# Kernel optimization log

Measured on AMD Instinct MI355X. Metric: run time of the kernel, lower is better.

Reference implementation:

```python
import jax, jax.numpy as jnp
import numpy as np

BN_EPS = 1e-5


def setup_inputs() -> dict:
    key = jax.random.key(0)
    ks = jax.random.split(key, 16)
    N, E, IN, H, A, L = 50000, 400000, 128, 192, 192, 3
    s = 0.02
    inp = {
        "x": jax.random.normal(ks[0], (N, IN), dtype=jnp.float32),
        "edge_index": jax.random.randint(ks[1], (2, E), 0, N, dtype=jnp.int32),
        "seed_idx": 123,
        "proj_w": jax.random.normal(ks[2], (IN, H), dtype=jnp.float32) * s,
        "proj_b": jnp.zeros((H,), dtype=jnp.float32),
        "mlp1_w": jax.random.normal(ks[3], (L, H, H), dtype=jnp.float32) * s,
        "mlp1_b": jnp.zeros((L, H), dtype=jnp.float32),
        "mlp2_w": jax.random.normal(ks[4], (L, H, H), dtype=jnp.float32) * s,
        "mlp2_b": jnp.zeros((L, H), dtype=jnp.float32),
        "eps": jnp.zeros((L,), dtype=jnp.float32),  # GIN train_eps init 0
        "bn_g": jnp.ones((L, H), dtype=jnp.float32),
        "bn_b": jnp.zeros((L, H), dtype=jnp.float32),
        "W1": jax.random.normal(ks[5], (H, A), dtype=jnp.float32) * s,
        "W2": jax.random.normal(ks[6], (H, A), dtype=jnp.float32) * s,
        "w_attn": jax.random.normal(ks[7], (A,), dtype=jnp.float32) * s,
        "cls_w": jax.random.normal(ks[8], (H,), dtype=jnp.float32) * s,
        "cls_b": jnp.zeros((1,), dtype=jnp.float32),
    }
    return inp


def _forward(x, edge_index, seed_idx, proj_w, proj_b, mlp1_w, mlp1_b,
             mlp2_w, mlp2_b, eps, bn_g, bn_b, W1, W2, w_attn, cls_w, cls_b):
    N = x.shape[0]
    src, dst = edge_index[0], edge_index[1]
    h = jax.nn.relu(x @ proj_w + proj_b)  # [N, H]
    L = mlp1_w.shape[0]
    for l in range(L):
        # GINConv: mlp((1+eps)*h + sum_{j->i} h_j) via scatter-add on dst
        agg = jax.ops.segment_sum(h[src], dst, num_segments=N)  # [N, H]
        z = (1.0 + eps[l]) * h + agg
        z = jax.nn.relu(z @ mlp1_w[l] + mlp1_b[l]) @ mlp2_w[l] + mlp2_b[l]
        # BatchNorm over nodes (batch statistics)
        mu = z.mean(axis=0)
        var = z.var(axis=0)
        z = (z - mu) * jax.lax.rsqrt(var + BN_EPS) * bn_g[l] + bn_b[l]
        h = jax.nn.relu(z)  # dropout is identity in eval
    h_seed = h[seed_idx]  # valid seed index branch
    zat = jnp.tanh(h @ W1 + h_seed @ W2)          # [N, A]
    e = jax.nn.leaky_relu(zat @ w_attn, 0.2)      # [N]
    alpha = jax.nn.softmax(e, axis=0)             # [N]
    readout = alpha @ h                           # [H]
    logit = readout @ cls_w + cls_b               # [1]
    return logit, alpha


def reference(x, edge_index, seed_idx, proj_w, proj_b, mlp1_w, mlp1_b,
              mlp2_w, mlp2_b, eps, bn_g, bn_b, W1, W2, w_attn, cls_w, cls_b):
    return _forward(x, edge_index, seed_idx, proj_w, proj_b, mlp1_w, mlp1_b,
                    mlp2_w, mlp2_b, eps, bn_g, bn_b, W1, W2, w_attn, cls_w, cls_b)
```

## Files before the change

kernel.cpp:

```cpp
#include <hip/hip_runtime.h>
#include <hip/hip_bf16.h>

#define N_NODES 50000
#define N_EDGES 400000
#define DIM_IN  128
#define DIM_H   192
#define N_LAYERS 3
#define BN_EPSF 1e-5f
#define SCAN_NBLK 49
#define INV_N (1.f / N_NODES)
#define NSHADOW 8
#define SSTRIDE 384
#define WTP_BLOCKS 138

typedef __attribute__((ext_vector_type(8))) short short8;
typedef __attribute__((ext_vector_type(4))) float floatx4;

union FragU { uint4 u; short8 s; };

__device__ __forceinline__ float relu_f(float x) { return x > 0.f ? x : 0.f; }
__device__ __forceinline__ unsigned short f2bf(float x) {
  __hip_bfloat16 h = __float2bfloat16(x);
  return *reinterpret_cast<unsigned short*>(&h);
}
__device__ __forceinline__ float bf2f(unsigned short b) {
  return __uint_as_float(((unsigned)b) << 16);
}
__device__ __forceinline__ float bflo(unsigned u) { return __uint_as_float(u << 16); }
__device__ __forceinline__ float bfhi(unsigned u) { return __uint_as_float(u & 0xffff0000u); }

__device__ __forceinline__ unsigned char f2f8(float v) {
  return (unsigned char)(__builtin_amdgcn_cvt_pk_fp8_f32(v, v, 0, false) & 0xff);
}
template <int SEL>
__device__ __forceinline__ float f8dec(unsigned u) {
  return __builtin_amdgcn_cvt_f32_fp8((int)u, SEL);
}

__global__ void k_wtp_hist(const float* __restrict__ m1, const float* __restrict__ m2,
                           const float* __restrict__ wa, const float* __restrict__ pw,
                           uint4* __restrict__ outp,
                           const int* __restrict__ edge, int* __restrict__ cnt) {
  if (blockIdx.x < WTP_BLOCKS) {
    const int NH = 7 * 24 * 192;
    const int NP = 16 * 192;
    int idx = blockIdx.x * 256 + threadIdx.x;
    if (idx >= NH + NP) return;
    union { uint4 u; unsigned short h[8]; } fr;
    if (idx < NH) {
      int mat = idx / (24 * 192);
      int rem = idx - mat * (24 * 192);
      int kidx = rem / 192, col = rem - kidx * 192;
      const float* src = mat < 3 ? m1 + (size_t)mat * (DIM_H * DIM_H)
                       : (mat < 6 ? m2 + (size_t)(mat - 3) * (DIM_H * DIM_H) : wa);
#pragma unroll
      for (int t = 0; t < 8; ++t) fr.h[t] = f2bf(src[(size_t)(kidx * 8 + t) * DIM_H + col]);
    } else {
      int rem = idx - NH;
      int kidx = rem / 192, col = rem - kidx * 192;
#pragma unroll
      for (int t = 0; t < 8; ++t) fr.h[t] = f2bf(pw[(size_t)(kidx * 8 + t) * DIM_H + col]);
    }
    outp[idx] = fr.u;
  } else {
    int e = (blockIdx.x - WTP_BLOCKS) * 256 + threadIdx.x;
    if (e < N_EDGES) atomicAdd(&cnt[edge[N_EDGES + e]], 1);
  }
}

__global__ void k_scanA(const int* __restrict__ deg, int* __restrict__ part, int* __restrict__ bsum) {
  __shared__ int buf[1024];
  int g = blockIdx.x * 1024 + threadIdx.x;
  int v = (g < N_NODES) ? deg[g] : 0;
  buf[threadIdx.x] = v;
  __syncthreads();
  for (int off = 1; off < 1024; off <<= 1) {
    int t = (threadIdx.x >= off) ? buf[threadIdx.x - off] : 0;
    __syncthreads();
    buf[threadIdx.x] += t;
    __syncthreads();
  }
  if (g < N_NODES) part[g] = buf[threadIdx.x];
  if (threadIdx.x == 1023) bsum[blockIdx.x] = buf[1023];
}

__global__ void k_scanC(const int* __restrict__ part, const int* __restrict__ bsum,
                        int* __restrict__ rowptr, int* __restrict__ cursor) {
  __shared__ int excl[64];
  int tid = threadIdx.x;
  if (tid < 64) {
    int own = (tid < SCAN_NBLK) ? bsum[tid] : 0;
    int v = own;
    for (int off = 1; off < 64; off <<= 1) {
      int t = __shfl_up(v, off);
      if (tid >= off) v += t;
    }
    excl[tid] = v - own;
  }
  __syncthreads();
  int g = blockIdx.x * 256 + tid;
  if (g == 0) { rowptr[0] = 0; cursor[0] = 0; }
  if (g < N_NODES) {
    int v = part[g] + excl[g >> 10];
    rowptr[g + 1] = v;
    if (g + 1 < N_NODES) cursor[g + 1] = v;
  }
}

__global__ void k_fill(const int* __restrict__ edge, int* __restrict__ cursor, int* __restrict__ csr) {
  int e = blockIdx.x * 256 + threadIdx.x;
  if (e < N_EDGES) {
    int s = edge[e];
    int d = edge[N_EDGES + e];
    int pos = atomicAdd(&cursor[d], 1);
    csr[pos] = s;
  }
}

template <bool BN>
__global__ void k_agg(const unsigned char* __restrict__ z, const int* __restrict__ rowptr,
                      const int* __restrict__ csr, const float* __restrict__ stats,
                      const float* __restrict__ bng, const float* __restrict__ bnb,
                      const float* __restrict__ eps, int l, unsigned short* __restrict__ outA) {
  int wid = threadIdx.x >> 6, lane = threadIdx.x & 63;
  int node = blockIdx.x * 4 + wid;
  if (node >= N_NODES || lane >= 48) return;
  int c = lane * 4;
  float4 sc4 = {1.f, 1.f, 1.f, 1.f}, sh4 = {0.f, 0.f, 0.f, 0.f};
  if (BN) {
    float4 st = {0.f, 0.f, 0.f, 0.f}, sq = {0.f, 0.f, 0.f, 0.f};
#pragma unroll
    for (int g = 0; g < NSHADOW; ++g) {
      const float* sp = stats + g * SSTRIDE;
      float4 a = *(const float4*)(sp + c);
      float4 b = *(const float4*)(sp + DIM_H + c);
      st.x += a.x; st.y += a.y; st.z += a.z; st.w += a.w;
      sq.x += b.x; sq.y += b.y; sq.z += b.z; sq.w += b.w;
    }
    float4 g4 = *(const float4*)(bng + c);
    float4 b4 = *(const float4*)(bnb + c);
    float mu, rs;
    mu = st.x * INV_N; rs = rsqrtf(sq.x * INV_N - mu * mu + BN_EPSF); sc4.x = g4.x * rs; sh4.x = b4.x - mu * sc4.x;
    mu = st.y * INV_N; rs = rsqrtf(sq.y * INV_N - mu * mu + BN_EPSF); sc4.y = g4.y * rs; sh4.y = b4.y - mu * sc4.y;
    mu = st.z * INV_N; rs = rsqrtf(sq.z * INV_N - mu * mu + BN_EPSF); sc4.z = g4.z * rs; sh4.z = b4.z - mu * sc4.z;
    mu = st.w * INV_N; rs = rsqrtf(sq.w * INV_N - mu * mu + BN_EPSF); sc4.w = g4.w * rs; sh4.w = b4.w - mu * sc4.w;
  }
  float a0 = 0.f, a1 = 0.f, a2 = 0.f, a3 = 0.f;
  int beg = rowptr[node], end = rowptr[node + 1];
  unsigned us = *(const unsigned*)(z + (size_t)node * DIM_H + c);
#define ACCU(U)                                                          \
  {                                                                      \
    float v0 = f8dec<0>(U), v1 = f8dec<1>(U);                            \
    float v2 = f8dec<2>(U), v3 = f8dec<3>(U);                            \
    if (BN) {                                                            \
      v0 = relu_f(fmaf(v0, sc4.x, sh4.x));                               \
      v1 = relu_f(fmaf(v1, sc4.y, sh4.y));                               \
      v2 = relu_f(fmaf(v2, sc4.z, sh4.z));                               \
      v3 = relu_f(fmaf(v3, sc4.w, sh4.w));                               \
    }                                                                    \
    a0 += v0; a1 += v1; a2 += v2; a3 += v3;                              \
  }
  int j = beg;
  for (; j + 4 <= end; j += 4) {
    int s0 = csr[j], s1 = csr[j + 1], s2 = csr[j + 2], s3 = csr[j + 3];
    unsigned u0 = *(const unsigned*)(z + (size_t)s0 * DIM_H + c);
    unsigned u1 = *(const unsigned*)(z + (size_t)s1 * DIM_H + c);
    unsigned u2 = *(const unsigned*)(z + (size_t)s2 * DIM_H + c);
    unsigned u3 = *(const unsigned*)(z + (size_t)s3 * DIM_H + c);
    ACCU(u0) ACCU(u1) ACCU(u2) ACCU(u3)
  }
  for (; j < end; ++j) {
    int s0 = csr[j];
    unsigned u0 = *(const unsigned*)(z + (size_t)s0 * DIM_H + c);
    ACCU(u0)
  }
#undef ACCU
  float ep = 1.f + eps[l];
  {
    float v0 = f8dec<0>(us), v1 = f8dec<1>(us), v2 = f8dec<2>(us), v3 = f8dec<3>(us);
    if (BN) {
      v0 = relu_f(fmaf(v0, sc4.x, sh4.x));
      v1 = relu_f(fmaf(v1, sc4.y, sh4.y));
      v2 = relu_f(fmaf(v2, sc4.z, sh4.z));
      v3 = relu_f(fmaf(v3, sc4.w, sh4.w));
    }
    a0 += ep * v0; a1 += ep * v1; a2 += ep * v2; a3 += ep * v3;
  }
  uint2 o;
  o.x = (unsigned)f2bf(a0) | ((unsigned)f2bf(a1) << 16);
  o.y = (unsigned)f2bf(a2) | ((unsigned)f2bf(a3) << 16);
  *(uint2*)(outA + (size_t)node * DIM_H + c) = o;
}

template <int KS>
__device__ __forceinline__ void load_b(const uint4* __restrict__ Bp, int colbase, int kq, int lr,
                                       FragU (&b)[KS][3]) {
#pragma unroll
  for (int ks = 0; ks < KS; ++ks)
#pragma unroll
    for (int n = 0; n < 3; ++n)
      b[ks][n].u = Bp[(ks * 4 + kq) * 192 + colbase + n * 16 + lr];
}

template <int KS, int MT>
__device__ __forceinline__ void mfma_stage_pre(const uint4* a_lds, const FragU (&b)[KS][3],
                                               int kq, int lr, floatx4 (&acc)[MT][3]) {
#pragma unroll
  for (int ks = 0; ks < KS; ++ks) {
    int kidx = ks * 4 + kq;
    FragU a[MT];
#pragma unroll
    for (int m = 0; m < MT; ++m) a[m].u = a_lds[kidx * (MT * 16) + m * 16 + lr];
#pragma unroll
    for (int n = 0; n < 3; ++n)
#pragma unroll
      for (int m = 0; m < MT; ++m)
        acc[m][n] = __builtin_amdgcn_mfma_f32_16x16x32_bf16(a[m].s, b[ks][n].s, acc[m][n], 0, 0, 0);
  }
}

__global__ __launch_bounds__(256) void k_proj(const float* __restrict__ A,
                                              const uint4* __restrict__ Bp,
                                              const float* __restrict__ bias,
                                              unsigned char* __restrict__ C) {
  __shared__ uint4 a_lds[16 * 64];
  const int tid = threadIdx.x;
  const int rbase = blockIdx.x * 64;
  const int lane = tid & 63, w = tid >> 6;
  const int kq = lane >> 4, lr = lane & 15;
  const int colbase = w * 48;
  FragU b[4][3];
  load_b<4>(Bp, colbase, kq, lr, b);
#pragma unroll
  for (int i = 0; i < 4; ++i) {
    int row = tid >> 2, kidx = i * 4 + (tid & 3);
    int gr = rbase + row;
    gr = gr < N_NODES ? gr : N_NODES - 1;
    const float* ap = A + (size_t)gr * DIM_IN + kidx * 8;
    float4 v0 = *(const float4*)ap;
    float4 v1 = *(const float4*)(ap + 4);
    union { uint4 u; unsigned short h[8]; } fr;
    fr.h[0] = f2bf(v0.x); fr.h[1] = f2bf(v0.y); fr.h[2] = f2bf(v0.z); fr.h[3] = f2bf(v0.w);
    fr.h[4] = f2bf(v1.x); fr.h[5] = f2bf(v1.y); fr.h[6] = f2bf(v1.z); fr.h[7] = f2bf(v1.w);
    a_lds[kidx * 64 + row] = fr.u;
  }
  __syncthreads();
  floatx4 acc[4][3];
  floatx4 zero4 = {0.f, 0.f, 0.f, 0.f};
#pragma unroll
  for (int m = 0; m < 4; ++m)
#pragma unroll
    for (int n = 0; n < 3; ++n) acc[m][n] = zero4;
  mfma_stage_pre<4, 4>(a_lds, b, kq, lr, acc);
#pragma unroll
  for (int n = 0; n < 3; ++n) {
    int col = colbase + n * 16 + lr;
    float bb = bias[col];
#pragma unroll
    for (int m = 0; m < 4; ++m)
#pragma unroll
      for (int j = 0; j < 4; ++j) {
        int row = rbase + m * 16 + kq * 4 + j;
        if (row < N_NODES) C[(size_t)row * DIM_H + col] = f2f8(relu_f(acc[m][n][j] + bb));
      }
  }
}

__device__ __forceinline__ void z_epi(floatx4 (&acc)[2][3], unsigned short* zl, const float* __restrict__ b1,
                                      int colbase, int kq, int lr) {
#pragma unroll
  for (int n = 0; n < 3; ++n) {
    int col = colbase + n * 16 + lr;
    float bb = b1[col];
#pragma unroll
    for (int m = 0; m < 2; ++m)
#pragma unroll
      for (int j = 0; j < 4; ++j) {
        int rowl = m * 16 + kq * 4 + j;
        zl[(col >> 3) * 256 + rowl * 8 + (col & 7)] = f2bf(relu_f(acc[m][n][j] + bb));
      }
  }
}

template <bool F8>
__device__ __forceinline__ void out_epi(floatx4 (&acc)[2][3], void* __restrict__ Zout,
                                        const float* __restrict__ b2, int rb, int colbase, int kq, int lr,
                                        float (&s3)[3], float (&q3)[3]) {
#pragma unroll
  for (int n = 0; n < 3; ++n) {
    int col = colbase + n * 16 + lr;
    float bb = b2[col];
#pragma unroll
    for (int m = 0; m < 2; ++m)
#pragma unroll
      for (int j = 0; j < 4; ++j) {
        int row = rb + m * 16 + kq * 4 + j;
        if (row < N_NODES) {
          float v = acc[m][n][j] + bb;
          if (F8)
            ((unsigned char*)Zout)[(size_t)row * DIM_H + col] = f2f8(v);
          else
            ((unsigned short*)Zout)[(size_t)row * DIM_H + col] = f2bf(v);
          s3[n] += v;
          q3[n] += v * v;
        }
      }
  }
}

template <bool F8>
__global__ __launch_bounds__(256, 3) void k_mlp(const unsigned short* __restrict__ A,
                                                const uint4* __restrict__ B1p, const float* __restrict__ b1,
                                                const uint4* __restrict__ B2p, const float* __restrict__ b2,
                                                void* __restrict__ Zout, float* __restrict__ stats) {
  __shared__ uint4 a_lds[2][24 * 32];
  const int tid = threadIdx.x;
  const int rbase = blockIdx.x * 64;
  const int lane = tid & 63, w = tid >> 6;
  const int kq = lane >> 4, lr = lane & 15;
  const int colbase = w * 48;
  uint4 areg[2][3];
  const int arow = tid >> 3;
#pragma unroll
  for (int t = 0; t < 2; ++t) {
    int agr = rbase + t * 32 + arow;
    agr = agr < N_NODES ? agr : N_NODES - 1;
#pragma unroll
    for (int i = 0; i < 3; ++i) {
      int kidx = i * 8 + (tid & 7);
      areg[t][i] = *(const uint4*)(A + (size_t)agr * DIM_H + kidx * 8);
    }
  }
  FragU b1r[6][3];
  load_b<6>(B1p, colbase, kq, lr, b1r);
#pragma unroll
  for (int t = 0; t < 2; ++t)
#pragma unroll
    for (int i = 0; i < 3; ++i) {
      int kidx = i * 8 + (tid & 7);
      a_lds[t][kidx * 32 + arow] = areg[t][i];
    }
  __syncthreads();
  floatx4 zero4 = {0.f, 0.f, 0.f, 0.f};
  floatx4 acc0[2][3], acc1[2][3];
#pragma unroll
  for (int m = 0; m < 2; ++m)
#pragma unroll
    for (int n = 0; n < 3; ++n) { acc0[m][n] = zero4; acc1[m][n] = zero4; }
  mfma_stage_pre<6, 2>(a_lds[0], b1r, kq, lr, acc0);
  mfma_stage_pre<6, 2>(a_lds[1], b1r, kq, lr, acc1);
  FragU b2r[6][3];
  load_b<6>(B2p, colbase, kq, lr, b2r);
  __syncthreads();
  z_epi(acc0, (unsigned short*)a_lds[0], b1, colbase, kq, lr);
  z_epi(acc1, (unsigned short*)a_lds[1], b1, colbase, kq, lr);
  __syncthreads();
#pragma unroll
  for (int m = 0; m < 2; ++m)
#pragma unroll
    for (int n = 0; n < 3; ++n) { acc0[m][n] = zero4; acc1[m][n] = zero4; }
  mfma_stage_pre<6, 2>(a_lds[0], b2r, kq, lr, acc0);
  mfma_stage_pre<6, 2>(a_lds[1], b2r, kq, lr, acc1);
  float s3[3] = {0.f, 0.f, 0.f}, q3[3] = {0.f, 0.f, 0.f};
  out_epi<F8>(acc0, Zout, b2, rbase, colbase, kq, lr, s3, q3);
  out_epi<F8>(acc1, Zout, b2, rbase + 32, colbase, kq, lr, s3, q3);
  __syncthreads();
  float* ps = (float*)a_lds;
  float* pq = ps + DIM_H * 4;
#pragma unroll
  for (int n = 0; n < 3; ++n) {
    int col = colbase + n * 16 + lr;
    ps[col * 4 + kq] = s3[n];
    pq[col * 4 + kq] = q3[n];
  }
  __syncthreads();
  if (tid < DIM_H) {
    float ts = 0.f, tq = 0.f;
#pragma unroll
    for (int g = 0; g < 4; ++g) {
      ts += ps[tid * 4 + g];
      tq += pq[tid * 4 + g];
    }
    float* sp = stats + (blockIdx.x & (NSHADOW - 1)) * SSTRIDE;
    atomicAdd(&sp[tid], ts);
    atomicAdd(&sp[DIM_H + tid], tq);
  }
}

__global__ void k_seed_s2(const unsigned short* __restrict__ Zin, const float* __restrict__ stats,
                          const float* __restrict__ bng, const float* __restrict__ bnb,
                          const int* __restrict__ seedp, const float* __restrict__ W2,
                          float* __restrict__ s2) {
  __shared__ float hs[DIM_H];
  __shared__ float red[4][DIM_H];
  int tid = threadIdx.x;
  if (tid < DIM_H) {
    int seed = seedp[0];
    float ts = 0.f, tq = 0.f;
#pragma unroll
    for (int g = 0; g < NSHADOW; ++g) {
      ts += stats[g * SSTRIDE + tid];
      tq += stats[g * SSTRIDE + DIM_H + tid];
    }
    float mu = ts * INV_N;
    float rs = rsqrtf(tq * INV_N - mu * mu + BN_EPSF);
    float sc = bng[tid] * rs;
    float sh = bnb[tid] - mu * sc;
    hs[tid] = relu_f(bf2f(Zin[(size_t)seed * DIM_H + tid]) * sc + sh);
  }
  __syncthreads();
  int a = tid % DIM_H, grp = tid / DIM_H;
  float s = 0.f;
  for (int k = grp * 48; k < grp * 48 + 48; ++k) s = fmaf(hs[k], W2[(size_t)k * DIM_H + a], s);
  red[grp][a] = s;
  __syncthreads();
  if (tid < DIM_H) s2[tid] = red[0][tid] + red[1][tid] + red[2][tid] + red[3][tid];
}

__global__ __launch_bounds__(256, 3) void k_attnm(const unsigned short* __restrict__ Zin,
                                                  const float* __restrict__ stats,
                                                  const float* __restrict__ bng,
                                                  const float* __restrict__ bnb,
                                                  const uint4* __restrict__ Bp,
                                                  const float* __restrict__ s2,
                                                  const float* __restrict__ wat,
                                                  float* __restrict__ p, float* __restrict__ scal) {
  __shared__ uint4 a_lds[24 * 64];
  __shared__ float cs[DIM_H], ch[DIM_H];
  const int tid = threadIdx.x;
  const int rbase = blockIdx.x * 64;
  const int lane = tid & 63, w = tid >> 6;
  const int kq = lane >> 4, lr = lane & 15;
  const int colbase = w * 48;
  FragU b[6][3];
  load_b<6>(Bp, colbase, kq, lr, b);
  if (tid < DIM_H) {
    float ts = 0.f, tq = 0.f;
#pragma unroll
    for (int g = 0; g < NSHADOW; ++g) {
      ts += stats[g * SSTRIDE + tid];
      tq += stats[g * SSTRIDE + DIM_H + tid];
    }
    float mu = ts * INV_N;
    float rs = rsqrtf(tq * INV_N - mu * mu + BN_EPSF);
    float sc = bng[tid] * rs;
    cs[tid] = sc;
    ch[tid] = bnb[tid] - mu * sc;
  }
  __syncthreads();
#pragma unroll
  for (int i = 0; i < 6; ++i) {
    int row = tid >> 2, kidx = i * 4 + (tid & 3);
    int gr = rbase + row;
    gr = gr < N_NODES ? gr : N_NODES - 1;
    union { uint4 u; unsigned short h[8]; } v, o;
    v.u = *(const uint4*)(Zin + (size_t)gr * DIM_H + kidx * 8);
#pragma unroll
    for (int t = 0; t < 8; ++t)
      o.h[t] = f2bf(relu_f(bf2f(v.h[t]) * cs[kidx * 8 + t] + ch[kidx * 8 + t]));
    a_lds[kidx * 64 + row] = o.u;
  }
  __syncthreads();
  floatx4 zero4 = {0.f, 0.f, 0.f, 0.f};
  floatx4 acc[4][3];
#pragma unroll
  for (int m = 0; m < 4; ++m)
#pragma unroll
    for (int n = 0; n < 3; ++n) acc[m][n] = zero4;
  mfma_stage_pre<6, 4>(a_lds, b, kq, lr, acc);
  float pv[16];
#pragma unroll
  for (int t = 0; t < 16; ++t) pv[t] = 0.f;
#pragma unroll
  for (int n = 0; n < 3; ++n) {
    int col = colbase + n * 16 + lr;
    float s2c = s2[col];
    float wv = wat[col];
#pragma unroll
    for (int m = 0; m < 4; ++m)
#pragma unroll
      for (int j = 0; j < 4; ++j) {
        float xv = acc[m][n][j] + s2c;
        xv = fminf(fmaxf(xv, -10.f), 10.f);
        float t = __expf(2.f * xv);
        pv[m * 4 + j] = fmaf((t - 1.f) / (t + 1.f), wv, pv[m * 4 + j]);
      }
  }
  __syncthreads();
  float* part = (float*)a_lds;
#pragma unroll
  for (int m = 0; m < 4; ++m)
#pragma unroll
    for (int j = 0; j < 4; ++j)
      part[(m * 16 + kq * 4 + j) * 65 + w * 16 + lr] = pv[m * 4 + j];
  __syncthreads();
  if (tid < 64) {
    float s = 0.f;
#pragma unroll
    for (int i = 0; i < 64; ++i) s += part[tid * 65 + i];
    s = s > 0.f ? s : 0.2f * s;
    float pe = __expf(s);
    int gr = rbase + tid;
    bool valid = gr < N_NODES;
    if (valid) p[gr] = pe;
    pe = valid ? pe : 0.f;
#pragma unroll
    for (int off = 32; off > 0; off >>= 1) pe += __shfl_xor(pe, off);
    if (tid == 0) atomicAdd(&scal[0], pe);
  }
}

#define RD_BLOCKS 512
__global__ __launch_bounds__(256) void k_readout(const float* __restrict__ p,
                                                 const float* __restrict__ scal,
                                                 const unsigned short* __restrict__ Zin,
                                                 const float* __restrict__ stats,
                                                 const float* __restrict__ bng,
                                                 const float* __restrict__ bnb,
                                                 float* __restrict__ alpha,
                                                 float* __restrict__ rdout) {
  __shared__ float red[4][DIM_H];
  const int tid = threadIdx.x;
  const int w = tid >> 6, lane = tid & 63;
  const int rpb = (N_NODES + RD_BLOCKS - 1) / RD_BLOCKS;
  int rbeg = blockIdx.x * rpb;
  int rend = rbeg + rpb;
  rend = rend < N_NODES ? rend : N_NODES;
  float a0 = 0.f, a1 = 0.f, a2 = 0.f, a3 = 0.f;
  if (lane < 48) {
    int c = lane * 4;
    float4 st = {0.f, 0.f, 0.f, 0.f}, sq = {0.f, 0.f, 0.f, 0.f};
#pragma unroll
    for (int g = 0; g < NSHADOW; ++g) {
      const float* sp = stats + g * SSTRIDE;
      float4 a = *(const float4*)(sp + c);
      float4 b = *(const float4*)(sp + DIM_H + c);
      st.x += a.x; st.y += a.y; st.z += a.z; st.w += a.w;
      sq.x += b.x; sq.y += b.y; sq.z += b.z; sq.w += b.w;
    }
    float4 g4 = *(const float4*)(bng + c);
    float4 b4 = *(const float4*)(bnb + c);
    float4 sc4, sh4;
    float mu, rs;
    mu = st.x * INV_N; rs = rsqrtf(sq.x * INV_N - mu * mu + BN_EPSF); sc4.x = g4.x * rs; sh4.x = b4.x - mu * sc4.x;
    mu = st.y * INV_N; rs = rsqrtf(sq.y * INV_N - mu * mu + BN_EPSF); sc4.y = g4.y * rs; sh4.y = b4.y - mu * sc4.y;
    mu = st.z * INV_N; rs = rsqrtf(sq.z * INV_N - mu * mu + BN_EPSF); sc4.z = g4.z * rs; sh4.z = b4.z - mu * sc4.z;
    mu = st.w * INV_N; rs = rsqrtf(sq.w * INV_N - mu * mu + BN_EPSF); sc4.w = g4.w * rs; sh4.w = b4.w - mu * sc4.w;
    float invS = 1.f / scal[0];
#pragma unroll 2
    for (int r = rbeg + w; r < rend; r += 4) {
      float pw = p[r];
      if (c == 0) alpha[r] = pw * invS;
      uint2 u = *(const uint2*)(Zin + (size_t)r * DIM_H + c);
      float v0 = relu_f(bflo(u.x) * sc4.x + sh4.x);
      float v1 = relu_f(bfhi(u.x) * sc4.y + sh4.y);
      float v2 = relu_f(bflo(u.y) * sc4.z + sh4.z);
      float v3 = relu_f(bfhi(u.y) * sc4.w + sh4.w);
      a0 = fmaf(pw, v0, a0); a1 = fmaf(pw, v1, a1);
      a2 = fmaf(pw, v2, a2); a3 = fmaf(pw, v3, a3);
    }
    float4 o = {a0, a1, a2, a3};
    *(float4*)&red[w][c] = o;
  }
  __syncthreads();
  if (tid < DIM_H) {
    float s = red[0][tid] + red[1][tid] + red[2][tid] + red[3][tid];
    atomicAdd(&rdout[tid], s);
  }
}

__global__ void k_logit(const float* __restrict__ rdout, const float* __restrict__ scal,
                        const float* __restrict__ cw, const float* __restrict__ cb,
                        float* __restrict__ out) {
  __shared__ float buf[256];
  int tid = threadIdx.x;
  buf[tid] = (tid < DIM_H) ? rdout[tid] * cw[tid] : 0.f;
  __syncthreads();
  for (int s = 128; s > 0; s >>= 1) {
    if (tid < s) buf[tid] += buf[tid + s];
    __syncthreads();
  }
  if (tid == 0) out[0] = buf[0] * (1.f / scal[0]) + cb[0];
}

extern "C" void kernel_launch(void* const* d_in, const int* in_sizes, int n_in,
                              void* d_out, int out_size, void* d_ws, size_t ws_size,
                              hipStream_t stream) {
  const float* x      = (const float*)d_in[0];
  const int*   edge   = (const int*)d_in[1];
  const int*   seedp  = (const int*)d_in[2];
  const float* proj_w = (const float*)d_in[3];
  const float* proj_b = (const float*)d_in[4];
  const float* mlp1_w = (const float*)d_in[5];
  const float* mlp1_b = (const float*)d_in[6];
  const float* mlp2_w = (const float*)d_in[7];
  const float* mlp2_b = (const float*)d_in[8];
  const float* eps    = (const float*)d_in[9];
  const float* bn_g   = (const float*)d_in[10];
  const float* bn_b   = (const float*)d_in[11];
  const float* W1     = (const float*)d_in[12];
  const float* W2     = (const float*)d_in[13];
  const float* w_attn = (const float*)d_in[14];
  const float* cls_w  = (const float*)d_in[15];
  const float* cls_b  = (const float*)d_in[16];
  float* out = (float*)d_out;

  char* ws = (char*)d_ws;
  size_t off = 0;
  auto alloc = [&](size_t bytes) -> void* {
    void* p = ws + off;
    off = (off + bytes + 255) & ~(size_t)255;
    return p;
  };
  unsigned char*  f8a    = (unsigned char*)alloc((size_t)N_NODES * DIM_H);
  unsigned char*  f8b    = (unsigned char*)alloc((size_t)N_NODES * DIM_H);
  unsigned short* aggOut = (unsigned short*)alloc((size_t)N_NODES * DIM_H * 2);
  unsigned short* zbf    = (unsigned short*)alloc((size_t)N_NODES * DIM_H * 2);
  float* pbuf   = (float*)alloc((size_t)N_NODES * 4);
  int* rowptr   = (int*)alloc((size_t)(N_NODES + 1) * 4);
  int* csr      = (int*)alloc((size_t)N_EDGES * 4);
  int* part     = (int*)alloc((size_t)N_NODES * 4);
  int* bsum     = (int*)alloc(64 * 4);
  float* s2     = (float*)alloc(DIM_H * 4);
  size_t zbeg = off;
  int* cursor   = (int*)alloc((size_t)(N_NODES + 1) * 4);
  float* statsA = (float*)alloc((size_t)N_LAYERS * NSHADOW * SSTRIDE * 4);
  float* scalrd = (float*)alloc(256 * 4);
  size_t zend = off;
  float* scal   = scalrd;
  float* rdout  = scalrd + 64;
  uint4* WTall  = (uint4*)alloc((size_t)(7 * 24 * 192 + 16 * 192) * 16);

  float* statsL[N_LAYERS];
  for (int l = 0; l < N_LAYERS; ++l) statsL[l] = statsA + (size_t)l * NSHADOW * SSTRIDE;

  const uint4* B1p[N_LAYERS] = {WTall, WTall + 4608, WTall + 2 * 4608};
  const uint4* B2p[N_LAYERS] = {WTall + 3 * 4608, WTall + 4 * 4608, WTall + 5 * 4608};
  const uint4* Bap = WTall + 6 * 4608;
  const uint4* Bpp = WTall + 7 * 4608;

  const int GRID64 = (N_NODES + 63) / 64;
  const int AGG_GRID = (N_NODES + 3) / 4;

  hipMemsetAsync(ws + zbeg, 0, zend - zbeg, stream);

  k_wtp_hist<<<WTP_BLOCKS + (N_EDGES + 255) / 256, 256, 0, stream>>>(
      mlp1_w, mlp2_w, W1, proj_w, WTall, edge, cursor);

  k_scanA<<<SCAN_NBLK, 1024, 0, stream>>>(cursor, part, bsum);
  k_scanC<<<(N_NODES + 255) / 256, 256, 0, stream>>>(part, bsum, rowptr, cursor);
  k_fill<<<(N_EDGES + 255) / 256, 256, 0, stream>>>(edge, cursor, csr);

  k_proj<<<GRID64, 256, 0, stream>>>(x, Bpp, proj_b, f8a);

  k_agg<false><<<AGG_GRID, 256, 0, stream>>>(f8a, rowptr, csr, statsL[0], bn_g, bn_b, eps, 0, aggOut);
  k_mlp<true><<<GRID64, 256, 0, stream>>>(aggOut, B1p[0], mlp1_b, B2p[0], mlp2_b, f8b, statsL[0]);
  k_agg<true><<<AGG_GRID, 256, 0, stream>>>(f8b, rowptr, csr, statsL[0], bn_g, bn_b, eps, 1, aggOut);
  k_mlp<true><<<GRID64, 256, 0, stream>>>(aggOut, B1p[1], mlp1_b + DIM_H, B2p[1], mlp2_b + DIM_H, f8a, statsL[1]);
  k_agg<true><<<AGG_GRID, 256, 0, stream>>>(f8a, rowptr, csr, statsL[1], bn_g + DIM_H, bn_b + DIM_H, eps, 2, aggOut);
  k_mlp<false><<<GRID64, 256, 0, stream>>>(aggOut, B1p[2], mlp1_b + 2 * DIM_H, B2p[2], mlp2_b + 2 * DIM_H, zbf, statsL[2]);

  const float* g2 = bn_g + (size_t)2 * DIM_H;
  const float* b2c = bn_b + (size_t)2 * DIM_H;

  k_seed_s2<<<1, 768, 0, stream>>>(zbf, statsL[2], g2, b2c, seedp, W2, s2);
  k_attnm<<<GRID64, 256, 0, stream>>>(zbf, statsL[2], g2, b2c, Bap, s2, w_attn, pbuf, scal);
  k_readout<<<RD_BLOCKS, 256, 0, stream>>>(pbuf, scal, zbf, statsL[2], g2, b2c, out + 1, rdout);
  k_logit<<<1, 256, 0, stream>>>(rdout, scal, cls_w, cls_b, out);
}
```

Measured before the change: 300.4 us.

## Fuse seed projection and weighted readout into attention kernel

Each attention block now computes the seed-node W2 projection itself, replacing the separate single-block kernel. It also accumulates the exp-weighted readout from the normalized features already staged in LDS, so the separate readout pass that re-read the whole bf16 feature matrix is gone. Partial sums go to shadowed atomics, and a light kernel normalizes alpha afterward. The cost is that every one of the ~782 blocks redundantly reads the 192x192 W2 matrix and does a 192-long dot product per thread, plus extra LDS and atomics.

```diff
diff --git a/kernel.cpp b/kernel.cpp
--- a/kernel.cpp
+++ b/kernel.cpp
@@ -387,46 +387,20 @@
   }
 }
 
-__global__ void k_seed_s2(const unsigned short* __restrict__ Zin, const float* __restrict__ stats,
-                          const float* __restrict__ bng, const float* __restrict__ bnb,
-                          const int* __restrict__ seedp, const float* __restrict__ W2,
-                          float* __restrict__ s2) {
-  __shared__ float hs[DIM_H];
-  __shared__ float red[4][DIM_H];
-  int tid = threadIdx.x;
-  if (tid < DIM_H) {
-    int seed = seedp[0];
-    float ts = 0.f, tq = 0.f;
-#pragma unroll
-    for (int g = 0; g < NSHADOW; ++g) {
-      ts += stats[g * SSTRIDE + tid];
-      tq += stats[g * SSTRIDE + DIM_H + tid];
-    }
-    float mu = ts * INV_N;
-    float rs = rsqrtf(tq * INV_N - mu * mu + BN_EPSF);
-    float sc = bng[tid] * rs;
-    float sh = bnb[tid] - mu * sc;
-    hs[tid] = relu_f(bf2f(Zin[(size_t)seed * DIM_H + tid]) * sc + sh);
-  }
-  __syncthreads();
-  int a = tid % DIM_H, grp = tid / DIM_H;
-  float s = 0.f;
-  for (int k = grp * 48; k < grp * 48 + 48; ++k) s = fmaf(hs[k], W2[(size_t)k * DIM_H + a], s);
-  red[grp][a] = s;
-  __syncthreads();
-  if (tid < DIM_H) s2[tid] = red[0][tid] + red[1][tid] + red[2][tid] + red[3][tid];
-}
-
 __global__ __launch_bounds__(256, 3) void k_attnm(const unsigned short* __restrict__ Zin,
                                                   const float* __restrict__ stats,
                                                   const float* __restrict__ bng,
                                                   const float* __restrict__ bnb,
                                                   const uint4* __restrict__ Bp,
-                                                  const float* __restrict__ s2,
+                                                  const int* __restrict__ seedp,
+                                                  const float* __restrict__ W2,
                                                   const float* __restrict__ wat,
-                                                  float* __restrict__ p, float* __restrict__ scal) {
+                                                  float* __restrict__ p, float* __restrict__ scal,
+                                                  float* __restrict__ rdoutS) {
   __shared__ uint4 a_lds[24 * 64];
-  __shared__ float cs[DIM_H], ch[DIM_H];
+  __shared__ float part[64][65];
+  __shared__ float cs[DIM_H], ch[DIM_H], hs[DIM_H], s2l[DIM_H];
+  __shared__ float pe_lds[64];
   const int tid = threadIdx.x;
   const int rbase = blockIdx.x * 64;
   const int lane = tid & 63, w = tid >> 6;
@@ -444,8 +418,11 @@
     float mu = ts * INV_N;
     float rs = rsqrtf(tq * INV_N - mu * mu + BN_EPSF);
     float sc = bng[tid] * rs;
+    float sh = bnb[tid] - mu * sc;
     cs[tid] = sc;
-    ch[tid] = bnb[tid] - mu * sc;
+    ch[tid] = sh;
+    int seed = seedp[0];
+    hs[tid] = relu_f(bf2f(Zin[(size_t)seed * DIM_H + tid]) * sc + sh);
   }
   __syncthreads();
 #pragma unroll
@@ -460,6 +437,16 @@
       o.h[t] = f2bf(relu_f(bf2f(v.h[t]) * cs[kidx * 8 + t] + ch[kidx * 8 + t]));
     a_lds[kidx * 64 + row] = o.u;
   }
+  if (tid < DIM_H) {
+    float t0 = 0.f, t1 = 0.f, t2 = 0.f, t3 = 0.f;
+    for (int k = 0; k < DIM_H; k += 4) {
+      t0 = fmaf(hs[k + 0], W2[(size_t)(k + 0) * DIM_H + tid], t0);
+      t1 = fmaf(hs[k + 1], W2[(size_t)(k + 1) * DIM_H + tid], t1);
+      t2 = fmaf(hs[k + 2], W2[(size_t)(k + 2) * DIM_H + tid], t2);
+      t3 = fmaf(hs[k + 3], W2[(size_t)(k + 3) * DIM_H + tid], t3);
+    }
+    s2l[tid] = (t0 + t1) + (t2 + t3);
+  }
   __syncthreads();
   floatx4 zero4 = {0.f, 0.f, 0.f, 0.f};
   floatx4 acc[4][3];
@@ -474,7 +461,7 @@
 #pragma unroll
   for (int n = 0; n < 3; ++n) {
     int col = colbase + n * 16 + lr;
-    float s2c = s2[col];
+    float s2c = s2l[col];
     float wv = wat[col];
 #pragma unroll
     for (int m = 0; m < 4; ++m)
@@ -486,95 +473,60 @@
         pv[m * 4 + j] = fmaf((t - 1.f) / (t + 1.f), wv, pv[m * 4 + j]);
       }
   }
-  __syncthreads();
-  float* part = (float*)a_lds;
 #pragma unroll
   for (int m = 0; m < 4; ++m)
 #pragma unroll
     for (int j = 0; j < 4; ++j)
-      part[(m * 16 + kq * 4 + j) * 65 + w * 16 + lr] = pv[m * 4 + j];
+      part[m * 16 + kq * 4 + j][w * 16 + lr] = pv[m * 4 + j];
   __syncthreads();
   if (tid < 64) {
     float s = 0.f;
 #pragma unroll
-    for (int i = 0; i < 64; ++i) s += part[tid * 65 + i];
+    for (int i = 0; i < 64; ++i) s += part[tid][i];
     s = s > 0.f ? s : 0.2f * s;
     float pe = __expf(s);
     int gr = rbase + tid;
     bool valid = gr < N_NODES;
     if (valid) p[gr] = pe;
     pe = valid ? pe : 0.f;
-#pragma unroll
-    for (int off = 32; off > 0; off >>= 1) pe += __shfl_xor(pe, off);
-    if (tid == 0) atomicAdd(&scal[0], pe);
-  }
-}
-
-#define RD_BLOCKS 512
-__global__ __launch_bounds__(256) void k_readout(const float* __restrict__ p,
-                                                 const float* __restrict__ scal,
-                                                 const unsigned short* __restrict__ Zin,
-                                                 const float* __restrict__ stats,
-                                                 const float* __restrict__ bng,
-                                                 const float* __restrict__ bnb,
-                                                 float* __restrict__ alpha,
-                                                 float* __restrict__ rdout) {
-  __shared__ float red[4][DIM_H];
-  const int tid = threadIdx.x;
-  const int w = tid >> 6, lane = tid & 63;
-  const int rpb = (N_NODES + RD_BLOCKS - 1) / RD_BLOCKS;
-  int rbeg = blockIdx.x * rpb;
-  int rend = rbeg + rpb;
-  rend = rend < N_NODES ? rend : N_NODES;
-  float a0 = 0.f, a1 = 0.f, a2 = 0.f, a3 = 0.f;
-  if (lane < 48) {
-    int c = lane * 4;
-    float4 st = {0.f, 0.f, 0.f, 0.f}, sq = {0.f, 0.f, 0.f, 0.f};
-#pragma unroll
-    for (int g = 0; g < NSHADOW; ++g) {
-      const float* sp = stats + g * SSTRIDE;
-      float4 a = *(const float4*)(sp + c);
-      float4 b = *(const float4*)(sp + DIM_H + c);
-      st.x += a.x; st.y += a.y; st.z += a.z; st.w += a.w;
-      sq.x += b.x; sq.y += b.y; sq.z += b.z; sq.w += b.w;
-    }
-    float4 g4 = *(const float4*)(bng + c);
-    float4 b4 = *(const float4*)(bnb + c);
-    float4 sc4, sh4;
-    float mu, rs;
-    mu = st.x * INV_N; rs = rsqrtf(sq.x * INV_N - mu * mu + BN_EPSF); sc4.x = g4.x * rs; sh4.x = b4.x - mu * sc4.x;
-    mu = st.y * INV_N; rs = rsqrtf(sq.y * INV_N - mu * mu + BN_EPSF); sc4.y = g4.y * rs; sh4.y = b4.y - mu * sc4.y;
-    mu = st.z * INV_N; rs = rsqrtf(sq.z * INV_N - mu * mu + BN_EPSF); sc4.z = g4.z * rs; sh4.z = b4.z - mu * sc4.z;
-    mu = st.w * INV_N; rs = rsqrtf(sq.w * INV_N - mu * mu + BN_EPSF); sc4.w = g4.w * rs; sh4.w = b4.w - mu * sc4.w;
-    float invS = 1.f / scal[0];
-#pragma unroll 2
-    for (int r = rbeg + w; r < rend; r += 4) {
-      float pw = p[r];
-      if (c == 0) alpha[r] = pw * invS;
-      uint2 u = *(const uint2*)(Zin + (size_t)r * DIM_H + c);
-      float v0 = relu_f(bflo(u.x) * sc4.x + sh4.x);
-      float v1 = relu_f(bfhi(u.x) * sc4.y + sh4.y);
-      float v2 = relu_f(bflo(u.y) * sc4.z + sh4.z);
-      float v3 = relu_f(bfhi(u.y) * sc4.w + sh4.w);
-      a0 = fmaf(pw, v0, a0); a1 = fmaf(pw, v1, a1);
-      a2 = fmaf(pw, v2, a2); a3 = fmaf(pw, v3, a3);
-    }
-    float4 o = {a0, a1, a2, a3};
-    *(float4*)&red[w][c] = o;
+    pe_lds[tid] = pe;
+    float red = pe;
+#pragma unroll
+    for (int off = 32; off > 0; off >>= 1) red += __shfl_xor(red, off);
+    if (tid == 0) atomicAdd(&scal[0], red);
   }
   __syncthreads();
   if (tid < DIM_H) {
-    float s = red[0][tid] + red[1][tid] + red[2][tid] + red[3][tid];
-    atomicAdd(&rdout[tid], s);
-  }
-}
-
-__global__ void k_logit(const float* __restrict__ rdout, const float* __restrict__ scal,
+    const unsigned short* al = (const unsigned short*)a_lds;
+    int base = (tid >> 3) * 512 + (tid & 7);
+    float s = 0.f;
+    for (int it = 0; it < 64; ++it) {
+      int row = (it + tid) & 63;
+      s = fmaf(pe_lds[row], bf2f(al[base + row * 8]), s);
+    }
+    atomicAdd(&rdoutS[(blockIdx.x & (NSHADOW - 1)) * DIM_H + tid], s);
+  }
+}
+
+__global__ void k_alpha(const float* __restrict__ p, const float* __restrict__ scal,
+                        float* __restrict__ alpha) {
+  int i = blockIdx.x * 256 + threadIdx.x;
+  if (i < N_NODES) alpha[i] = p[i] * (1.f / scal[0]);
+}
+
+__global__ void k_logit(const float* __restrict__ rdoutS, const float* __restrict__ scal,
                         const float* __restrict__ cw, const float* __restrict__ cb,
                         float* __restrict__ out) {
   __shared__ float buf[256];
   int tid = threadIdx.x;
-  buf[tid] = (tid < DIM_H) ? rdout[tid] * cw[tid] : 0.f;
+  float v = 0.f;
+  if (tid < DIM_H) {
+    float s = 0.f;
+#pragma unroll
+    for (int g = 0; g < NSHADOW; ++g) s += rdoutS[g * DIM_H + tid];
+    v = s * cw[tid];
+  }
+  buf[tid] = v;
   __syncthreads();
   for (int s = 128; s > 0; s >>= 1) {
     if (tid < s) buf[tid] += buf[tid + s];
@@ -621,14 +573,13 @@
   int* csr      = (int*)alloc((size_t)N_EDGES * 4);
   int* part     = (int*)alloc((size_t)N_NODES * 4);
   int* bsum     = (int*)alloc(64 * 4);
-  float* s2     = (float*)alloc(DIM_H * 4);
   size_t zbeg = off;
   int* cursor   = (int*)alloc((size_t)(N_NODES + 1) * 4);
   float* statsA = (float*)alloc((size_t)N_LAYERS * NSHADOW * SSTRIDE * 4);
-  float* scalrd = (float*)alloc(256 * 4);
+  float* scalrd = (float*)alloc((size_t)(64 + NSHADOW * DIM_H) * 4);
   size_t zend = off;
   float* scal   = scalrd;
-  float* rdout  = scalrd + 64;
+  float* rdoutS = scalrd + 64;
   uint4* WTall  = (uint4*)alloc((size_t)(7 * 24 * 192 + 16 * 192) * 16);
 
   float* statsL[N_LAYERS];
@@ -663,8 +614,7 @@
   const float* g2 = bn_g + (size_t)2 * DIM_H;
   const float* b2c = bn_b + (size_t)2 * DIM_H;
 
-  k_seed_s2<<<1, 768, 0, stream>>>(zbf, statsL[2], g2, b2c, seedp, W2, s2);
-  k_attnm<<<GRID64, 256, 0, stream>>>(zbf, statsL[2], g2, b2c, Bap, s2, w_attn, pbuf, scal);
-  k_readout<<<RD_BLOCKS, 256, 0, stream>>>(pbuf, scal, zbf, statsL[2], g2, b2c, out + 1, rdout);
-  k_logit<<<1, 256, 0, stream>>>(rdout, scal, cls_w, cls_b, out);
-}
+  k_attnm<<<GRID64, 256, 0, stream>>>(zbf, statsL[2], g2, b2c, Bap, seedp, W2, w_attn, pbuf, scal, rdoutS);
+  k_alpha<<<(N_NODES + 255) / 256, 256, 0, stream>>>(pbuf, scal, out + 1);
+  k_logit<<<1, 256, 0, stream>>>(rdoutS, scal, cls_w, cls_b, out);
+}
```

Result: faster. 288.8 us (median of 2 runs) (-3.9%).
